# Performance work log

Hardware: AMD Instinct MI355X
Metric: run time of the kernel (lower is better)

## Reference

```python
import jax, jax.numpy as jnp
import numpy as np

B, T, D, N = 4, 1024, 1024, 16


def setup_inputs() -> dict:
    key = jax.random.key(0)
    ks = jax.random.split(key, 16)
    s = 1.0 / np.sqrt(D)
    inp = {
        "u": jax.random.normal(ks[0], (B, T, D), jnp.float32),
        "Win": jax.random.normal(ks[1], (D, D), jnp.float32) * s,
        "b_in": jnp.zeros((D,), jnp.float32),
        "Wg": jax.random.normal(ks[2], (D, D), jnp.float32) * s,
        "bg": jnp.zeros((D,), jnp.float32),
        "Wout": jax.random.normal(ks[3], (D, D), jnp.float32) * s,
        "bout": jnp.zeros((D,), jnp.float32),
        "convw": jax.random.normal(ks[4], (D, 3), jnp.float32) * 0.5,  # depthwise k=3
        "convb": jnp.zeros((D,), jnp.float32),
        "A": -jnp.exp(jax.random.normal(ks[5], (D, N), jnp.float32) * 0.5),  # negative diag
        "Wb": jax.random.normal(ks[6], (D, N), jnp.float32) * s,
        "bb": jnp.zeros((N,), jnp.float32),
        "Wc": jax.random.normal(ks[7], (D, N), jnp.float32) * s,
        "bc": jnp.zeros((N,), jnp.float32),
        "Wdt": jax.random.normal(ks[8], (D, D), jnp.float32) * s,
        "bdt": jnp.full((D,), -2.0, jnp.float32),  # small initial dt after softplus
    }
    return inp


def _depthwise_conv3_same(x, w, b):
    # x: [B,T,D], w: [D,3], b: [D]; Conv1d(k=3, padding=1, groups=D)
    xp = jnp.pad(x, ((0, 0), (1, 1), (0, 0)))
    return xp[:, :-2] * w[:, 0] + xp[:, 1:-1] * w[:, 1] + xp[:, 2:] * w[:, 2] + b


def _selective_scan(x, A, Wb, bb, Wc, bc, Wdt, bdt):
    # x: [B,T,D]
    dt = jax.nn.softplus(x @ Wdt + bdt)            # [B,T,D]
    Bm = x @ Wb + bb                               # [B,T,N]
    Cm = x @ Wc + bc                               # [B,T,N]
    dA = jnp.exp(dt[..., None] * A)                # [B,T,D,N]
    dBx = dt[..., None] * Bm[:, :, None, :] * x[..., None]  # [B,T,D,N]

    def step(h, ins):
        dA_t, dBx_t, C_t = ins                     # [B,D,N],[B,D,N],[B,N]
        h = dA_t * h + dBx_t
        y = jnp.einsum('bdn,bn->bd', h, C_t)
        return h, y

    h0 = jnp.zeros((x.shape[0], x.shape[2], A.shape[1]), x.dtype)
    _, ys = jax.lax.scan(
        step, h0,
        (dA.transpose(1, 0, 2, 3), dBx.transpose(1, 0, 2, 3), Cm.transpose(1, 0, 2)))
    return ys.transpose(1, 0, 2)                   # [B,T,D]


def reference(u, Win, b_in, Wg, bg, Wout, bout, convw, convb, A, Wb, bb, Wc, bc, Wdt, bdt):
    x = u @ Win + b_in                             # in_proj
    x = _depthwise_conv3_same(x, convw, convb)     # depthwise conv, same padding
    x = jax.nn.silu(x)
    x_ssm = _selective_scan(x, A, Wb, bb, Wc, bc, Wdt, bdt)
    z = jax.nn.silu(u @ Wg + bg)                   # gate
    return (x_ssm * z) @ Wout + bout
```

## Files before the change

### kernel.cpp

```cpp
#include <hip/hip_runtime.h>
#include <hip/hip_bf16.h>
#include <math.h>

#define BB 4
#define TT 1024
#define DD 1024
#define NNs 16
#define MM (BB*TT)
#define MMDD ((size_t)MM*DD)
#define CHUNK 64
#define NCHUNK (TT/CHUNK)

typedef short bf16x8 __attribute__((ext_vector_type(8)));
typedef float f32x4  __attribute__((ext_vector_type(4)));

__device__ __forceinline__ float silu_f(float v)     { return v / (1.f + __expf(-v)); }
__device__ __forceinline__ float softplus_f(float v) { return fmaxf(v, 0.f) + log1pf(__expf(-fabsf(v))); }

__device__ __forceinline__ unsigned short f2bf(float f) {
  unsigned u = __builtin_bit_cast(unsigned, f);
  u += 0x7fffu + ((u >> 16) & 1u);
  return (unsigned short)(u >> 16);
}
__device__ __forceinline__ unsigned pk2(float a, float b) {
  return (unsigned)f2bf(a) | ((unsigned)f2bf(b) << 16);
}

__device__ __forceinline__ void gload16(const void* g, void* l) {
  __builtin_amdgcn_global_load_lds(
      (const __attribute__((address_space(1))) unsigned*)g,
      (__attribute__((address_space(3))) unsigned*)l, 16, 0, 0);
}

__device__ __forceinline__ int2 xcd_swz(int gx) {
  int nwg  = gx * (int)gridDim.y;
  int orig = (int)blockIdx.y * gx + (int)blockIdx.x;
  int q = nwg >> 3, r = nwg & 7;
  int xcd = orig & 7, i = orig >> 3;
  int wg = (xcd < r ? xcd * (q + 1) : r * (q + 1) + (xcd - r) * q) + i;
  return make_int2(wg % gx, wg / gx);
}

__global__ __launch_bounds__(256) void wconv_t4(
    const float* __restrict__ W0, const float* __restrict__ W1,
    const float* __restrict__ W2, const float* __restrict__ W3,
    short* __restrict__ o0, short* __restrict__ o1,
    short* __restrict__ o2, short* __restrict__ o3)
{
  const float* W; short* Wt;
  switch (blockIdx.z) {
    case 0:  W = W0; Wt = o0; break;
    case 1:  W = W1; Wt = o1; break;
    case 2:  W = W2; Wt = o2; break;
    default: W = W3; Wt = o3; break;
  }
  __shared__ float t[32][33];
  int n0 = blockIdx.x * 32, k0 = blockIdx.y * 32;
  int r  = threadIdx.x >> 3;
  int c4 = (threadIdx.x & 7) * 4;
  float4 v = *(const float4*)(W + (size_t)(k0 + r) * DD + n0 + c4);
  t[r][c4+0] = v.x; t[r][c4+1] = v.y; t[r][c4+2] = v.z; t[r][c4+3] = v.w;
  __syncthreads();
  short q0 = (short)f2bf(t[c4+0][r]);
  short q1 = (short)f2bf(t[c4+1][r]);
  short q2 = (short)f2bf(t[c4+2][r]);
  short q3 = (short)f2bf(t[c4+3][r]);
  *(short4*)(Wt + (size_t)(n0 + r) * DD + k0 + c4) = make_short4(q0, q1, q2, q3);
}

__global__ __launch_bounds__(256) void wbc_t(
    const float* __restrict__ Wb, const float* __restrict__ Wc,
    short* __restrict__ Wbct)
{
  int idx = blockIdx.x * 256 + threadIdx.x;
  int k = idx & (DD - 1);
  int n = idx >> 10;
  const float* W = (n < 16) ? Wb : Wc;
  Wbct[(size_t)n * DD + k] = (short)f2bf(W[(size_t)k * NNs + (n & 15)]);
}

__global__ __launch_bounds__(256) void to_bf16(
    const float* __restrict__ in, short* __restrict__ out)
{
  size_t i = (size_t)(blockIdx.x * 256 + threadIdx.x) * 8;
  float4 a = *(const float4*)(in + i);
  float4 b = *(const float4*)(in + i + 4);
  *(uint4*)(out + i) = make_uint4(pk2(a.x,a.y), pk2(a.z,a.w),
                                  pk2(b.x,b.y), pk2(b.z,b.w));
}

__device__ __forceinline__ void gemm_core(
    const short* __restrict__ Ab, const short* __restrict__ Bt,
    const float* __restrict__ bias, float* __restrict__ C,
    int Nn, int K, int bm0, int bn0, int epi,
    short* As, short* Bs)
{
  const int tid  = threadIdx.x;
  const int lane = tid & 63;
  const int w    = tid >> 6;
  const int wm0  = (w >> 1) * 64;
  const int wn0  = (w & 1) * 64;

  const int srow = tid >> 3;
  const int scol = ((tid & 7) ^ ((tid >> 3) & 7)) << 3;

  const short* gA = Ab + (size_t)(bm0 + srow) * K + scol;
  const short* gB = Bt + (size_t)(bn0 + srow) * K + scol;
  char* ldsA = (char*)As;
  char* ldsB = (char*)Bs;
  const int wuni = w * 1024;

  f32x4 acc[4][4];
  const f32x4 zz = {0.f, 0.f, 0.f, 0.f};
  #pragma unroll
  for (int m = 0; m < 4; m++)
    #pragma unroll
    for (int n = 0; n < 4; n++) acc[m][n] = zz;

  const int fr  = lane & 15;
  const int ks  = (lane >> 4) << 3;
  const int swz = (fr & 7) << 3;

  const int NT = K >> 6;

  #pragma unroll
  for (int i = 0; i < 4; i++) {
    gload16(gA + (size_t)(i * 32) * K, ldsA + i * 4096 + wuni);
    gload16(gB + (size_t)(i * 32) * K, ldsB + i * 4096 + wuni);
  }
  __syncthreads();

  for (int t = 0; t < NT; ++t) {
    const int cur = t & 1;
    if (t + 1 < NT) {
      const int k1 = (t + 1) << 6;
      const int bo = (cur ^ 1) * 16384;
      #pragma unroll
      for (int i = 0; i < 4; i++) {
        gload16(gA + (size_t)(i * 32) * K + k1, ldsA + bo + i * 4096 + wuni);
        gload16(gB + (size_t)(i * 32) * K + k1, ldsB + bo + i * 4096 + wuni);
      }
    }
    const short* Ac = As + cur * 8192;
    const short* Bc = Bs + cur * 8192;
    #pragma unroll
    for (int s = 0; s < 2; s++) {
      const int cs = ((s << 5) | ks) ^ swz;
      bf16x8 af[4], bf[4];
      #pragma unroll
      for (int m = 0; m < 4; m++)
        af[m] = *(const bf16x8*)&Ac[(wm0 + m*16 + fr) * 64 + cs];
      #pragma unroll
      for (int n = 0; n < 4; n++)
        bf[n] = *(const bf16x8*)&Bc[(wn0 + n*16 + fr) * 64 + cs];
      #pragma unroll
      for (int m = 0; m < 4; m++)
        #pragma unroll
        for (int n = 0; n < 4; n++)
          acc[m][n] = __builtin_amdgcn_mfma_f32_16x16x32_bf16(af[m], bf[n], acc[m][n], 0, 0, 0);
    }
    __syncthreads();
  }

  const int orow = (lane >> 4) * 4;
  const int ocol = lane & 15;
  #pragma unroll
  for (int n = 0; n < 4; n++) {
    const int col = bn0 + wn0 + n*16 + ocol;
    const float bv = bias[col];
    #pragma unroll
    for (int m = 0; m < 4; m++) {
      #pragma unroll
      for (int r = 0; r < 4; r++) {
        float v = acc[m][n][r] + bv;
        if (epi == 1) v = silu_f(v);
        else if (epi == 2) v = softplus_f(v);
        C[(size_t)(bm0 + wm0 + m*16 + orow + r) * Nn + col] = v;
      }
    }
  }
}

__global__ __launch_bounds__(256) void gemm_bf16_k(
    const short* __restrict__ Ab, const short* __restrict__ Bt,
    const float* __restrict__ bias, float* __restrict__ C,
    int Nn, int K, int epi)
{
  __shared__ short As[2*128*64];
  __shared__ short Bs[2*128*64];
  int2 p = xcd_swz(gridDim.x);
  gemm_core(Ab, Bt, bias, C, Nn, K, p.y * 128, p.x * 128, epi, As, Bs);
}

__global__ __launch_bounds__(256) void gemm_ing_k(
    const short* __restrict__ ub,
    const short* __restrict__ Wti, const short* __restrict__ Wtg,
    const float* __restrict__ b_in, const float* __restrict__ bg,
    float* __restrict__ x1, float* __restrict__ z)
{
  __shared__ short As[2*128*64];
  __shared__ short Bs[2*128*64];
  int2 p = xcd_swz(gridDim.x);
  const int gate = p.x >> 3;
  gemm_core(ub, gate ? Wtg : Wti, gate ? bg : b_in, gate ? z : x1,
            DD, DD, p.y * 128, (p.x & 7) * 128, gate ? 1 : 0, As, Bs);
}

__global__ __launch_bounds__(256) void gemm_dtbc_k(
    const short* __restrict__ xb, const short* __restrict__ Wtd,
    const short* __restrict__ Wbct,
    const float* __restrict__ bdt, const float* __restrict__ bb,
    const float* __restrict__ bc,
    float* __restrict__ dt, float* __restrict__ Bm, float* __restrict__ Cm)
{
  __shared__ short As[2*128*64];
  __shared__ short Bs[2*128*64];
  __shared__ short Cs[2*32*64];
  int2 p = xcd_swz(gridDim.x);
  const int bx = p.x;
  const int bm0 = p.y * 128;
  const int bn0 = bx * 128;

  const int tid  = threadIdx.x;
  const int lane = tid & 63;
  const int w    = tid >> 6;
  const int wm0  = (w >> 1) * 64;
  const int wn0  = (w & 1) * 64;

  const int srow = tid >> 3;
  const int scol = ((tid & 7) ^ ((tid >> 3) & 7)) << 3;

  const short* gA = xb   + (size_t)(bm0 + srow) * DD + scol;
  const short* gB = Wtd  + (size_t)(bn0 + srow) * DD + scol;
  const short* gC = Wbct + (size_t)srow * DD + scol;
  char* ldsA = (char*)As;
  char* ldsB = (char*)Bs;
  char* ldsC = (char*)Cs;
  const int wuni = w * 1024;

  f32x4 acc[4][4];
  const f32x4 zz = {0.f, 0.f, 0.f, 0.f};
  #pragma unroll
  for (int m = 0; m < 4; m++)
    #pragma unroll
    for (int n = 0; n < 4; n++) acc[m][n] = zz;
  f32x4 accbc = zz;

  const int fr  = lane & 15;
  const int ks  = (lane >> 4) << 3;
  const int swz = (fr & 7) << 3;

  #pragma unroll
  for (int i = 0; i < 4; i++) {
    gload16(gA + (size_t)(i * 32) * DD, ldsA + i * 4096 + wuni);
    gload16(gB + (size_t)(i * 32) * DD, ldsB + i * 4096 + wuni);
  }
  gload16(gC, ldsC + wuni);
  __syncthreads();

  for (int t = 0; t < 16; ++t) {
    const int cur = t & 1;
    if (t + 1 < 16) {
      const int k1 = (t + 1) << 6;
      const int bo = (cur ^ 1) * 16384;
      #pragma unroll
      for (int i = 0; i < 4; i++) {
        gload16(gA + (size_t)(i * 32) * DD + k1, ldsA + bo + i * 4096 + wuni);
        gload16(gB + (size_t)(i * 32) * DD + k1, ldsB + bo + i * 4096 + wuni);
      }
      gload16(gC + k1, ldsC + (cur ^ 1) * 4096 + wuni);
    }
    const short* Ac = As + cur * 8192;
    const short* Bc = Bs + cur * 8192;
    const short* Cc = Cs + cur * 2048;
    #pragma unroll
    for (int s = 0; s < 2; s++) {
      const int cs = ((s << 5) | ks) ^ swz;
      bf16x8 af[4], bf[4];
      #pragma unroll
      for (int m = 0; m < 4; m++)
        af[m] = *(const bf16x8*)&Ac[(wm0 + m*16 + fr) * 64 + cs];
      #pragma unroll
      for (int n = 0; n < 4; n++)
        bf[n] = *(const bf16x8*)&Bc[(wn0 + n*16 + fr) * 64 + cs];
      #pragma unroll
      for (int m = 0; m < 4; m++)
        #pragma unroll
        for (int n = 0; n < 4; n++)
          acc[m][n] = __builtin_amdgcn_mfma_f32_16x16x32_bf16(af[m], bf[n], acc[m][n], 0, 0, 0);
      if (w < 2) {
        bf16x8 abc = *(const bf16x8*)&Ac[(bx*16 + fr) * 64 + cs];
        bf16x8 bbc = *(const bf16x8*)&Cc[((w << 4) + fr) * 64 + cs];
        accbc = __builtin_amdgcn_mfma_f32_16x16x32_bf16(abc, bbc, accbc, 0, 0, 0);
      }
    }
    __syncthreads();
  }

  const int orow = (lane >> 4) * 4;
  const int ocol = lane & 15;
  #pragma unroll
  for (int n = 0; n < 4; n++) {
    const int col = bn0 + wn0 + n*16 + ocol;
    const float bv = bdt[col];
    #pragma unroll
    for (int m = 0; m < 4; m++) {
      #pragma unroll
      for (int r = 0; r < 4; r++) {
        float v = acc[m][n][r] + bv;
        dt[(size_t)(bm0 + wm0 + m*16 + orow + r) * DD + col] = softplus_f(v);
      }
    }
  }
  if (w < 2) {
    const float bv = (w == 0 ? bb : bc)[ocol];
    float* dst = (w == 0) ? Bm : Cm;
    #pragma unroll
    for (int r = 0; r < 4; r++) {
      int row = bm0 + bx*16 + orow + r;
      dst[(size_t)row * NNs + ocol] = accbc[r] + bv;
    }
  }
}

__global__ __launch_bounds__(256) void conv_silu(
    const float* __restrict__ x1, const float* __restrict__ cw,
    const float* __restrict__ cb, float* __restrict__ x,
    short* __restrict__ xb)
{
  int idx = blockIdx.x * 256 + threadIdx.x;
  int d4 = idx & (DD/4 - 1);
  int bt = idx >> 8;
  int t  = bt & (TT - 1);
  const float4* b4 = (const float4*)x1;
  size_t ri = (size_t)bt * (DD/4) + d4;
  float4 zz = make_float4(0.f, 0.f, 0.f, 0.f);
  float4 vc = b4[ri];
  float4 vm = (t > 0)      ? b4[ri - DD/4] : zz;
  float4 vp = (t < TT - 1) ? b4[ri + DD/4] : zz;
  float rm[4] = {vm.x, vm.y, vm.z, vm.w};
  float rc[4] = {vc.x, vc.y, vc.z, vc.w};
  float rp[4] = {vp.x, vp.y, vp.z, vp.w};
  float o[4];
  #pragma unroll
  for (int j = 0; j < 4; j++) {
    int d = d4*4 + j;
    float v = rm[j]*cw[d*3+0] + rc[j]*cw[d*3+1] + rp[j]*cw[d*3+2] + cb[d];
    o[j] = silu_f(v);
  }
  ((float4*)x)[ri] = make_float4(o[0], o[1], o[2], o[3]);
  ((uint2*)xb)[ri] = make_uint2(pk2(o[0], o[1]), pk2(o[2], o[3]));
}

__global__ __launch_bounds__(256) void scan_local(
    const float* __restrict__ dt, const float* __restrict__ x,
    const float* __restrict__ Bm, const float* __restrict__ A,
    float* __restrict__ P, float* __restrict__ S)
{
  __shared__ float Bs[CHUNK*NNs];
  int bid = blockIdx.x;
  int dblk = bid & 3;
  int c = (bid >> 2) & 15;
  int b = bid >> 6;
  int d = dblk*256 + threadIdx.x;
  int t0 = c * CHUNK;
  for (int i = threadIdx.x; i < CHUNK*NNs; i += 256)
    Bs[i] = Bm[(size_t)(b*TT + t0)*NNs + i];
  float a[NNs];
  #pragma unroll
  for (int n = 0; n < NNs; n++) a[n] = A[d*NNs + n];
  __syncthreads();
  float h[NNs], p[NNs];
  #pragma unroll
  for (int n = 0; n < NNs; n++) { h[n] = 0.f; p[n] = 1.f; }
  size_t base = (size_t)(b*TT + t0)*DD + d;
  for (int tt = 0; tt < CHUNK; tt++) {
    float dtv = dt[base + (size_t)tt*DD];
    float xv  = x [base + (size_t)tt*DD];
    float dx = dtv * xv;
    #pragma unroll
    for (int n = 0; n < NNs; n++) {
      float e = __expf(dtv * a[n]);
      h[n] = fmaf(e, h[n], dx * Bs[tt*NNs + n]);
      p[n] *= e;
    }
  }
  size_t o = ((size_t)((b*NCHUNK + c)*DD + d)) * NNs;
  #pragma unroll
  for (int n = 0; n < NNs; n += 4) {
    *(float4*)&P[o+n] = make_float4(p[n], p[n+1], p[n+2], p[n+3]);
    *(float4*)&S[o+n] = make_float4(h[n], h[n+1], h[n+2], h[n+3]);
  }
}

__global__ __launch_bounds__(256) void scan_combine(
    const float* __restrict__ P, const float* __restrict__ S,
    float* __restrict__ H0)
{
  int g = blockIdx.x*256 + threadIdx.x;
  int n = g & 15; int d = (g >> 4) & 1023; int b = g >> 14;
  float h = 0.f;
  for (int c = 0; c < NCHUNK; c++) {
    size_t idx = ((size_t)((b*NCHUNK + c)*DD + d)) * NNs + n;
    H0[idx] = h;
    h = fmaf(P[idx], h, S[idx]);
  }
}

__global__ __launch_bounds__(256) void scan_y(
    const float* __restrict__ dt, const float* __restrict__ x,
    const float* __restrict__ Bm, const float* __restrict__ Cm,
    const float* __restrict__ A,  const float* __restrict__ H0,
    const float* __restrict__ z,  short* __restrict__ xsb)
{
  __shared__ float Bs[CHUNK*NNs];
  __shared__ float Cs[CHUNK*NNs];
  int bid = blockIdx.x;
  int dblk = bid & 3;
  int c = (bid >> 2) & 15;
  int b = bid >> 6;
  int d = dblk*256 + threadIdx.x;
  int t0 = c * CHUNK;
  for (int i = threadIdx.x; i < CHUNK*NNs; i += 256) {
    Bs[i] = Bm[(size_t)(b*TT + t0)*NNs + i];
    Cs[i] = Cm[(size_t)(b*TT + t0)*NNs + i];
  }
  float a[NNs];
  #pragma unroll
  for (int n = 0; n < NNs; n++) a[n] = A[d*NNs + n];
  size_t ho = ((size_t)((b*NCHUNK + c)*DD + d)) * NNs;
  float h[NNs];
  #pragma unroll
  for (int n = 0; n < NNs; n += 4) {
    float4 h4 = *(const float4*)&H0[ho+n];
    h[n] = h4.x; h[n+1] = h4.y; h[n+2] = h4.z; h[n+3] = h4.w;
  }
  __syncthreads();
  size_t base = (size_t)(b*TT + t0)*DD + d;
  for (int tt = 0; tt < CHUNK; tt++) {
    float dtv = dt[base + (size_t)tt*DD];
    float xv  = x [base + (size_t)tt*DD];
    float dx = dtv * xv;
    float y = 0.f;
    #pragma unroll
    for (int n = 0; n < NNs; n++) {
      float e = __expf(dtv * a[n]);
      h[n] = fmaf(e, h[n], dx * Bs[tt*NNs + n]);
      y = fmaf(h[n], Cs[tt*NNs + n], y);
    }
    size_t gi = base + (size_t)tt*DD;
    xsb[gi] = (short)f2bf(y * z[gi]);
  }
}

extern "C" void kernel_launch(void* const* d_in, const int* in_sizes, int n_in,
                              void* d_out, int out_size, void* d_ws, size_t ws_size,
                              hipStream_t stream)
{
  const float* u     = (const float*)d_in[0];
  const float* Win   = (const float*)d_in[1];
  const float* b_in  = (const float*)d_in[2];
  const float* Wg    = (const float*)d_in[3];
  const float* bg    = (const float*)d_in[4];
  const float* Wout  = (const float*)d_in[5];
  const float* bout  = (const float*)d_in[6];
  const float* convw = (const float*)d_in[7];
  const float* convb = (const float*)d_in[8];
  const float* A     = (const float*)d_in[9];
  const float* Wb    = (const float*)d_in[10];
  const float* bb    = (const float*)d_in[11];
  const float* Wc    = (const float*)d_in[12];
  const float* bc    = (const float*)d_in[13];
  const float* Wdt   = (const float*)d_in[14];
  const float* bdt   = (const float*)d_in[15];
  float* out = (float*)d_out;

  float* ws = (float*)d_ws;
  float* x1 = ws;
  float* z  = x1 + MMDD;
  float* x  = z  + MMDD;
  float* dt = x  + MMDD;
  float* Bm = dt + MMDD;
  float* Cm = Bm + (size_t)MM*NNs;
  short* ub  = (short*)(Cm + (size_t)MM*NNs);
  short* xb  = ub  + MMDD;
  short* Wti = xb  + MMDD;
  short* Wtg = Wti + (size_t)DD*DD;
  short* Wtd = Wtg + (size_t)DD*DD;
  short* Wto = Wtd + (size_t)DD*DD;
  short* Wbct = Wto + (size_t)DD*DD;
  float* P  = x1;
  float* S  = P + (size_t)BB*NCHUNK*DD*NNs;
  float* H0 = S + (size_t)BB*NCHUNK*DD*NNs;
  short* xsb = ub;

  wconv_t4<<<dim3(DD/32, DD/32, 4), 256, 0, stream>>>(
      Win, Wg, Wdt, Wout, Wti, Wtg, Wtd, Wto);
  wbc_t<<<(32*DD)/256, 256, 0, stream>>>(Wb, Wc, Wbct);
  to_bf16<<<(MMDD/8)/256, 256, 0, stream>>>(u, ub);

  gemm_ing_k<<<dim3(16, MM/128), 256, 0, stream>>>(ub, Wti, Wtg, b_in, bg, x1, z);
  conv_silu<<<(MMDD/4)/256, 256, 0, stream>>>(x1, convw, convb, x, xb);
  gemm_dtbc_k<<<dim3(8, MM/128), 256, 0, stream>>>(
      xb, Wtd, Wbct, bdt, bb, bc, dt, Bm, Cm);
  scan_local  <<<BB*NCHUNK*(DD/256), 256, 0, stream>>>(dt, x, Bm, A, P, S);
  scan_combine<<<(BB*DD*NNs)/256,    256, 0, stream>>>(P, S, H0);
  scan_y      <<<BB*NCHUNK*(DD/256), 256, 0, stream>>>(dt, x, Bm, Cm, A, H0, z, xsb);
  gemm_bf16_k<<<dim3(8, MM/128), 256, 0, stream>>>(xsb, Wto, bout, out, DD, DD, 0);
}
```

Measured before the change: 308.0 us.

## Triple-buffer GEMM LDS stages with vmcnt waits and one barrier per tile

Moves the bf16 GEMM kernels from double to triple LDS buffering, issuing loads two K-tiles ahead. Each iteration now does a partial s_waitcnt on vmcnt and a single s_barrier instead of two __syncthreads. The goal is to hide more global-to-LDS load latency and cut barrier stalls. In exchange, LDS use per block grows by half, which may lower occupancy, and correctness depends on the vmcnt counts matching the number of outstanding loads.

```diff
diff --git a/kernel.cpp b/kernel.cpp
--- a/kernel.cpp
+++ b/kernel.cpp
@@ -123,26 +123,27 @@
 
   const int NT = K >> 6;
 
-  #pragma unroll
-  for (int i = 0; i < 4; i++) {
-    gload16(gA + (size_t)(i * 32) * K, ldsA + i * 4096 + wuni);
-    gload16(gB + (size_t)(i * 32) * K, ldsB + i * 4096 + wuni);
-  }
-  __syncthreads();
+  auto STAGE = [&](int t) {
+    const int ko = t << 6;
+    const int bo = (t % 3) * 16384;
+    #pragma unroll
+    for (int i = 0; i < 4; i++) {
+      gload16(gA + (size_t)(i * 32) * K + ko, ldsA + bo + i * 4096 + wuni);
+      gload16(gB + (size_t)(i * 32) * K + ko, ldsB + bo + i * 4096 + wuni);
+    }
+  };
+
+  STAGE(0);
+  STAGE(1);
 
   for (int t = 0; t < NT; ++t) {
-    const int cur = t & 1;
-    if (t + 1 < NT) {
-      const int k1 = (t + 1) << 6;
-      const int bo = (cur ^ 1) * 16384;
-      #pragma unroll
-      for (int i = 0; i < 4; i++) {
-        gload16(gA + (size_t)(i * 32) * K + k1, ldsA + bo + i * 4096 + wuni);
-        gload16(gB + (size_t)(i * 32) * K + k1, ldsB + bo + i * 4096 + wuni);
-      }
-    }
-    const short* Ac = As + cur * 8192;
-    const short* Bc = Bs + cur * 8192;
+    if (t + 1 < NT) asm volatile("s_waitcnt vmcnt(8)" ::: "memory");
+    else            asm volatile("s_waitcnt vmcnt(0)" ::: "memory");
+    __builtin_amdgcn_s_barrier();
+    if (t + 2 < NT) STAGE(t + 2);
+
+    const short* Ac = As + (t % 3) * 8192;
+    const short* Bc = Bs + (t % 3) * 8192;
     #pragma unroll
     for (int s = 0; s < 2; s++) {
       const int cs = ((s << 5) | ks) ^ swz;
@@ -159,7 +160,6 @@
         for (int n = 0; n < 4; n++)
           acc[m][n] = __builtin_amdgcn_mfma_f32_16x16x32_bf16(af[m], bf[n], acc[m][n], 0, 0, 0);
     }
-    __syncthreads();
   }
 
   const int orow = (lane >> 4) * 4;
@@ -186,8 +186,8 @@
     const float* __restrict__ bias, float* __restrict__ C,
     int Nn, int K, int epi)
 {
-  __shared__ short As[2*128*64];
-  __shared__ short Bs[2*128*64];
+  __shared__ short As[3*128*64];
+  __shared__ short Bs[3*128*64];
   int2 p = xcd_swz(gridDim.x);
   gemm_core(Ab, Bt, bias, C, Nn, K, p.y * 128, p.x * 128, epi, As, Bs);
 }
@@ -198,8 +198,8 @@
     const float* __restrict__ b_in, const float* __restrict__ bg,
     float* __restrict__ x1, float* __restrict__ z)
 {
-  __shared__ short As[2*128*64];
-  __shared__ short Bs[2*128*64];
+  __shared__ short As[3*128*64];
+  __shared__ short Bs[3*128*64];
   int2 p = xcd_swz(gridDim.x);
   const int gate = p.x >> 3;
   gemm_core(ub, gate ? Wtg : Wti, gate ? bg : b_in, gate ? z : x1,
@@ -213,11 +213,11 @@
     const float* __restrict__ bc,
     float* __restrict__ dt, float* __restrict__ Bm, float* __restrict__ Cm)
 {
-  __shared__ short As[2*128*64];
-  __shared__ short Bs[2*128*64];
-  __shared__ short Cs[2*32*64];
+  __shared__ short As[3*128*64];
+  __shared__ short Bs[3*128*64];
+  __shared__ short Cs[3*32*64];
   int2 p = xcd_swz(gridDim.x);
-  const int bx = p.x;
+  const int bx  = p.x;
   const int bm0 = p.y * 128;
   const int bn0 = bx * 128;
 
@@ -250,29 +250,29 @@
   const int ks  = (lane >> 4) << 3;
   const int swz = (fr & 7) << 3;
 
-  #pragma unroll
-  for (int i = 0; i < 4; i++) {
-    gload16(gA + (size_t)(i * 32) * DD, ldsA + i * 4096 + wuni);
-    gload16(gB + (size_t)(i * 32) * DD, ldsB + i * 4096 + wuni);
-  }
-  gload16(gC, ldsC + wuni);
-  __syncthreads();
+  auto STAGE = [&](int t) {
+    const int ko = t << 6;
+    const int bo = (t % 3) * 16384;
+    #pragma unroll
+    for (int i = 0; i < 4; i++) {
+      gload16(gA + (size_t)(i * 32) * DD + ko, ldsA + bo + i * 4096 + wuni);
+      gload16(gB + (size_t)(i * 32) * DD + ko, ldsB + bo + i * 4096 + wuni);
+    }
+    gload16(gC + ko, ldsC + (t % 3) * 4096 + wuni);
+  };
+
+  STAGE(0);
+  STAGE(1);
 
   for (int t = 0; t < 16; ++t) {
-    const int cur = t & 1;
-    if (t + 1 < 16) {
-      const int k1 = (t + 1) << 6;
-      const int bo = (cur ^ 1) * 16384;
-      #pragma unroll
-      for (int i = 0; i < 4; i++) {
-        gload16(gA + (size_t)(i * 32) * DD + k1, ldsA + bo + i * 4096 + wuni);
-        gload16(gB + (size_t)(i * 32) * DD + k1, ldsB + bo + i * 4096 + wuni);
-      }
-      gload16(gC + k1, ldsC + (cur ^ 1) * 4096 + wuni);
-    }
-    const short* Ac = As + cur * 8192;
-    const short* Bc = Bs + cur * 8192;
-    const short* Cc = Cs + cur * 2048;
+    if (t + 1 < 16) asm volatile("s_waitcnt vmcnt(9)" ::: "memory");
+    else            asm volatile("s_waitcnt vmcnt(0)" ::: "memory");
+    __builtin_amdgcn_s_barrier();
+    if (t + 2 < 16) STAGE(t + 2);
+
+    const short* Ac = As + (t % 3) * 8192;
+    const short* Bc = Bs + (t % 3) * 8192;
+    const short* Cc = Cs + (t % 3) * 2048;
     #pragma unroll
     for (int s = 0; s < 2; s++) {
       const int cs = ((s << 5) | ks) ^ swz;
@@ -294,7 +294,6 @@
         accbc = __builtin_amdgcn_mfma_f32_16x16x32_bf16(abc, bbc, accbc, 0, 0, 0);
       }
     }
-    __syncthreads();
   }
 
   const int orow = (lane >> 4) * 4;
```

Result: slower. 317.4 us (+3.0%).

## Split-K the dt/BC and output GEMMs and fuse bias/softplus into scans

Applied to the files above, without the earlier changes.

The dt/B/C GEMM and the output GEMM now split K in two halves across blockIdx.z, doubling the number of workgroups from 256 to 512 so more compute units are filled. Partial sums are written to separate buffers. The scan kernels combine them and apply bias and softplus on the fly, and a new epilogue kernel adds the two output partials plus bias. The fp32 copy of x is dropped and the scans read the bf16 x instead, which cuts memory traffic but lowers the precision of x in the scan. In exchange there is an extra partial-buffer write and read for dt and the output, plus one more launch.

```diff
diff --git a/kernel.cpp b/kernel.cpp
--- a/kernel.cpp
+++ b/kernel.cpp
@@ -24,6 +24,9 @@
 }
 __device__ __forceinline__ unsigned pk2(float a, float b) {
   return (unsigned)f2bf(a) | ((unsigned)f2bf(b) << 16);
+}
+__device__ __forceinline__ float bf2f(short s) {
+  return __builtin_bit_cast(float, ((unsigned)(unsigned short)s) << 16);
 }
 
 __device__ __forceinline__ void gload16(const void* g, void* l) {
@@ -92,7 +95,7 @@
 __device__ __forceinline__ void gemm_core(
     const short* __restrict__ Ab, const short* __restrict__ Bt,
     const float* __restrict__ bias, float* __restrict__ C,
-    int Nn, int K, int bm0, int bn0, int epi,
+    int Nn, int K, int kBase, int kLen, int bm0, int bn0, int epi,
     short* As, short* Bs)
 {
   const int tid  = threadIdx.x;
@@ -104,8 +107,8 @@
   const int srow = tid >> 3;
   const int scol = ((tid & 7) ^ ((tid >> 3) & 7)) << 3;
 
-  const short* gA = Ab + (size_t)(bm0 + srow) * K + scol;
-  const short* gB = Bt + (size_t)(bn0 + srow) * K + scol;
+  const short* gA = Ab + (size_t)(bm0 + srow) * K + kBase + scol;
+  const short* gB = Bt + (size_t)(bn0 + srow) * K + kBase + scol;
   char* ldsA = (char*)As;
   char* ldsB = (char*)Bs;
   const int wuni = w * 1024;
@@ -121,7 +124,7 @@
   const int ks  = (lane >> 4) << 3;
   const int swz = (fr & 7) << 3;
 
-  const int NT = K >> 6;
+  const int NT = kLen >> 6;
 
   #pragma unroll
   for (int i = 0; i < 4; i++) {
@@ -167,7 +170,7 @@
   #pragma unroll
   for (int n = 0; n < 4; n++) {
     const int col = bn0 + wn0 + n*16 + ocol;
-    const float bv = bias[col];
+    const float bv = bias ? bias[col] : 0.f;
     #pragma unroll
     for (int m = 0; m < 4; m++) {
       #pragma unroll
@@ -181,17 +184,6 @@
   }
 }
 
-__global__ __launch_bounds__(256) void gemm_bf16_k(
-    const short* __restrict__ Ab, const short* __restrict__ Bt,
-    const float* __restrict__ bias, float* __restrict__ C,
-    int Nn, int K, int epi)
-{
-  __shared__ short As[2*128*64];
-  __shared__ short Bs[2*128*64];
-  int2 p = xcd_swz(gridDim.x);
-  gemm_core(Ab, Bt, bias, C, Nn, K, p.y * 128, p.x * 128, epi, As, Bs);
-}
-
 __global__ __launch_bounds__(256) void gemm_ing_k(
     const short* __restrict__ ub,
     const short* __restrict__ Wti, const short* __restrict__ Wtg,
@@ -203,23 +195,40 @@
   int2 p = xcd_swz(gridDim.x);
   const int gate = p.x >> 3;
   gemm_core(ub, gate ? Wtg : Wti, gate ? bg : b_in, gate ? z : x1,
-            DD, DD, p.y * 128, (p.x & 7) * 128, gate ? 1 : 0, As, Bs);
+            DD, DD, 0, DD, p.y * 128, (p.x & 7) * 128, gate ? 1 : 0, As, Bs);
+}
+
+__global__ __launch_bounds__(256) void gemm_out_k(
+    const short* __restrict__ xsb, const short* __restrict__ Wto,
+    float* __restrict__ O0, float* __restrict__ O1)
+{
+  __shared__ short As[2*128*64];
+  __shared__ short Bs[2*128*64];
+  int2 p = xcd_swz(gridDim.x);
+  const int s = blockIdx.z;
+  gemm_core(xsb, Wto, nullptr, s ? O1 : O0,
+            DD, DD, s * 512, 512, p.y * 128, p.x * 128, 0, As, Bs);
 }
 
 __global__ __launch_bounds__(256) void gemm_dtbc_k(
     const short* __restrict__ xb, const short* __restrict__ Wtd,
     const short* __restrict__ Wbct,
-    const float* __restrict__ bdt, const float* __restrict__ bb,
-    const float* __restrict__ bc,
-    float* __restrict__ dt, float* __restrict__ Bm, float* __restrict__ Cm)
+    float* __restrict__ d0, float* __restrict__ d1,
+    float* __restrict__ B0, float* __restrict__ B1,
+    float* __restrict__ C0, float* __restrict__ C1)
 {
   __shared__ short As[2*128*64];
   __shared__ short Bs[2*128*64];
   __shared__ short Cs[2*32*64];
   int2 p = xcd_swz(gridDim.x);
-  const int bx = p.x;
+  const int sp  = blockIdx.z;
+  const int kB  = sp * 512;
+  const int bx  = p.x;
   const int bm0 = p.y * 128;
   const int bn0 = bx * 128;
+  float* dOut = sp ? d1 : d0;
+  float* bOut = sp ? B1 : B0;
+  float* cOut = sp ? C1 : C0;
 
   const int tid  = threadIdx.x;
   const int lane = tid & 63;
@@ -230,9 +239,9 @@
   const int srow = tid >> 3;
   const int scol = ((tid & 7) ^ ((tid >> 3) & 7)) << 3;
 
-  const short* gA = xb   + (size_t)(bm0 + srow) * DD + scol;
-  const short* gB = Wtd  + (size_t)(bn0 + srow) * DD + scol;
-  const short* gC = Wbct + (size_t)srow * DD + scol;
+  const short* gA = xb   + (size_t)(bm0 + srow) * DD + kB + scol;
+  const short* gB = Wtd  + (size_t)(bn0 + srow) * DD + kB + scol;
+  const short* gC = Wbct + (size_t)srow * DD + kB + scol;
   char* ldsA = (char*)As;
   char* ldsB = (char*)Bs;
   char* ldsC = (char*)Cs;
@@ -258,9 +267,9 @@
   gload16(gC, ldsC + wuni);
   __syncthreads();
 
-  for (int t = 0; t < 16; ++t) {
+  for (int t = 0; t < 8; ++t) {
     const int cur = t & 1;
-    if (t + 1 < 16) {
+    if (t + 1 < 8) {
       const int k1 = (t + 1) << 6;
       const int bo = (cur ^ 1) * 16384;
       #pragma unroll
@@ -302,31 +311,26 @@
   #pragma unroll
   for (int n = 0; n < 4; n++) {
     const int col = bn0 + wn0 + n*16 + ocol;
-    const float bv = bdt[col];
     #pragma unroll
     for (int m = 0; m < 4; m++) {
       #pragma unroll
-      for (int r = 0; r < 4; r++) {
-        float v = acc[m][n][r] + bv;
-        dt[(size_t)(bm0 + wm0 + m*16 + orow + r) * DD + col] = softplus_f(v);
-      }
+      for (int r = 0; r < 4; r++)
+        dOut[(size_t)(bm0 + wm0 + m*16 + orow + r) * DD + col] = acc[m][n][r];
     }
   }
   if (w < 2) {
-    const float bv = (w == 0 ? bb : bc)[ocol];
-    float* dst = (w == 0) ? Bm : Cm;
+    float* dst = (w == 0) ? bOut : cOut;
     #pragma unroll
     for (int r = 0; r < 4; r++) {
       int row = bm0 + bx*16 + orow + r;
-      dst[(size_t)row * NNs + ocol] = accbc[r] + bv;
+      dst[(size_t)row * NNs + ocol] = accbc[r];
     }
   }
 }
 
 __global__ __launch_bounds__(256) void conv_silu(
     const float* __restrict__ x1, const float* __restrict__ cw,
-    const float* __restrict__ cb, float* __restrict__ x,
-    short* __restrict__ xb)
+    const float* __restrict__ cb, short* __restrict__ xb)
 {
   int idx = blockIdx.x * 256 + threadIdx.x;
   int d4 = idx & (DD/4 - 1);
@@ -348,40 +352,44 @@
     float v = rm[j]*cw[d*3+0] + rc[j]*cw[d*3+1] + rp[j]*cw[d*3+2] + cb[d];
     o[j] = silu_f(v);
   }
-  ((float4*)x)[ri] = make_float4(o[0], o[1], o[2], o[3]);
   ((uint2*)xb)[ri] = make_uint2(pk2(o[0], o[1]), pk2(o[2], o[3]));
 }
 
 __global__ __launch_bounds__(256) void scan_local(
-    const float* __restrict__ dt, const float* __restrict__ x,
-    const float* __restrict__ Bm, const float* __restrict__ A,
+    const float* __restrict__ d0, const float* __restrict__ d1,
+    const float* __restrict__ bdt, const short* __restrict__ xb,
+    const float* __restrict__ B0, const float* __restrict__ B1,
+    const float* __restrict__ bb, const float* __restrict__ A,
     float* __restrict__ P, float* __restrict__ S)
 {
-  __shared__ float Bs[CHUNK*NNs];
+  __shared__ float Bsh[CHUNK*NNs];
   int bid = blockIdx.x;
   int dblk = bid & 3;
   int c = (bid >> 2) & 15;
   int b = bid >> 6;
   int d = dblk*256 + threadIdx.x;
   int t0 = c * CHUNK;
+  size_t bo = (size_t)(b*TT + t0)*NNs;
   for (int i = threadIdx.x; i < CHUNK*NNs; i += 256)
-    Bs[i] = Bm[(size_t)(b*TT + t0)*NNs + i];
+    Bsh[i] = B0[bo + i] + B1[bo + i] + bb[i & 15];
   float a[NNs];
   #pragma unroll
   for (int n = 0; n < NNs; n++) a[n] = A[d*NNs + n];
+  const float bdtv = bdt[d];
   __syncthreads();
   float h[NNs], p[NNs];
   #pragma unroll
   for (int n = 0; n < NNs; n++) { h[n] = 0.f; p[n] = 1.f; }
   size_t base = (size_t)(b*TT + t0)*DD + d;
   for (int tt = 0; tt < CHUNK; tt++) {
-    float dtv = dt[base + (size_t)tt*DD];
-    float xv  = x [base + (size_t)tt*DD];
+    size_t gi = base + (size_t)tt*DD;
+    float dtv = softplus_f(d0[gi] + d1[gi] + bdtv);
+    float xv  = bf2f(xb[gi]);
     float dx = dtv * xv;
     #pragma unroll
     for (int n = 0; n < NNs; n++) {
       float e = __expf(dtv * a[n]);
-      h[n] = fmaf(e, h[n], dx * Bs[tt*NNs + n]);
+      h[n] = fmaf(e, h[n], dx * Bsh[tt*NNs + n]);
       p[n] *= e;
     }
   }
@@ -402,32 +410,39 @@
   float h = 0.f;
   for (int c = 0; c < NCHUNK; c++) {
     size_t idx = ((size_t)((b*NCHUNK + c)*DD + d)) * NNs + n;
+    float pv = P[idx], sv = S[idx];
     H0[idx] = h;
-    h = fmaf(P[idx], h, S[idx]);
+    h = fmaf(pv, h, sv);
   }
 }
 
 __global__ __launch_bounds__(256) void scan_y(
-    const float* __restrict__ dt, const float* __restrict__ x,
-    const float* __restrict__ Bm, const float* __restrict__ Cm,
+    const float* __restrict__ d0, const float* __restrict__ d1,
+    const float* __restrict__ bdt, const short* __restrict__ xb,
+    const float* __restrict__ B0, const float* __restrict__ B1,
+    const float* __restrict__ bb,
+    const float* __restrict__ C0, const float* __restrict__ C1,
+    const float* __restrict__ bc,
     const float* __restrict__ A,  const float* __restrict__ H0,
     const float* __restrict__ z,  short* __restrict__ xsb)
 {
-  __shared__ float Bs[CHUNK*NNs];
-  __shared__ float Cs[CHUNK*NNs];
+  __shared__ float Bsh[CHUNK*NNs];
+  __shared__ float Csh[CHUNK*NNs];
   int bid = blockIdx.x;
   int dblk = bid & 3;
   int c = (bid >> 2) & 15;
   int b = bid >> 6;
   int d = dblk*256 + threadIdx.x;
   int t0 = c * CHUNK;
+  size_t bo = (size_t)(b*TT + t0)*NNs;
   for (int i = threadIdx.x; i < CHUNK*NNs; i += 256) {
-    Bs[i] = Bm[(size_t)(b*TT + t0)*NNs + i];
-    Cs[i] = Cm[(size_t)(b*TT + t0)*NNs + i];
+    Bsh[i] = B0[bo + i] + B1[bo + i] + bb[i & 15];
+    Csh[i] = C0[bo + i] + C1[bo + i] + bc[i & 15];
   }
   float a[NNs];
   #pragma unroll
   for (int n = 0; n < NNs; n++) a[n] = A[d*NNs + n];
+  const float bdtv = bdt[d];
   size_t ho = ((size_t)((b*NCHUNK + c)*DD + d)) * NNs;
   float h[NNs];
   #pragma unroll
@@ -438,19 +453,32 @@
   __syncthreads();
   size_t base = (size_t)(b*TT + t0)*DD + d;
   for (int tt = 0; tt < CHUNK; tt++) {
-    float dtv = dt[base + (size_t)tt*DD];
-    float xv  = x [base + (size_t)tt*DD];
+    size_t gi = base + (size_t)tt*DD;
+    float dtv = softplus_f(d0[gi] + d1[gi] + bdtv);
+    float xv  = bf2f(xb[gi]);
     float dx = dtv * xv;
     float y = 0.f;
     #pragma unroll
     for (int n = 0; n < NNs; n++) {
       float e = __expf(dtv * a[n]);
-      h[n] = fmaf(e, h[n], dx * Bs[tt*NNs + n]);
-      y = fmaf(h[n], Cs[tt*NNs + n], y);
-    }
-    size_t gi = base + (size_t)tt*DD;
+      h[n] = fmaf(e, h[n], dx * Bsh[tt*NNs + n]);
+      y = fmaf(h[n], Csh[tt*NNs + n], y);
+    }
     xsb[gi] = (short)f2bf(y * z[gi]);
   }
+}
+
+__global__ __launch_bounds__(256) void out_epi(
+    const float* __restrict__ O0, const float* __restrict__ O1,
+    const float* __restrict__ bout, float* __restrict__ out)
+{
+  size_t i = (size_t)(blockIdx.x * 256 + threadIdx.x) * 4;
+  int col = (int)(i & (DD - 1));
+  float4 a = *(const float4*)(O0 + i);
+  float4 b = *(const float4*)(O1 + i);
+  float4 bv = *(const float4*)(bout + col);
+  *(float4*)(out + i) = make_float4(a.x + b.x + bv.x, a.y + b.y + bv.y,
+                                    a.z + b.z + bv.z, a.w + b.w + bv.w);
 }
 
 extern "C" void kernel_launch(void* const* d_in, const int* in_sizes, int n_in,
@@ -478,11 +506,13 @@
   float* ws = (float*)d_ws;
   float* x1 = ws;
   float* z  = x1 + MMDD;
-  float* x  = z  + MMDD;
-  float* dt = x  + MMDD;
-  float* Bm = dt + MMDD;
-  float* Cm = Bm + (size_t)MM*NNs;
-  short* ub  = (short*)(Cm + (size_t)MM*NNs);
+  float* d0 = z  + MMDD;
+  float* d1 = d0 + MMDD;
+  float* B0 = d1 + MMDD;
+  float* B1 = B0 + (size_t)MM*NNs;
+  float* C0 = B1 + (size_t)MM*NNs;
+  float* C1 = C0 + (size_t)MM*NNs;
+  short* ub  = (short*)(C1 + (size_t)MM*NNs);
   short* xb  = ub  + MMDD;
   short* Wti = xb  + MMDD;
   short* Wtg = Wti + (size_t)DD*DD;
@@ -491,7 +521,9 @@
   short* Wbct = Wto + (size_t)DD*DD;
   float* P  = x1;
   float* S  = P + (size_t)BB*NCHUNK*DD*NNs;
-  float* H0 = S + (size_t)BB*NCHUNK*DD*NNs;
+  float* H0 = P;
+  float* O0 = d0;
+  float* O1 = d1;
   short* xsb = ub;
 
   wconv_t4<<<dim3(DD/32, DD/32, 4), 256, 0, stream>>>(
@@ -500,11 +532,14 @@
   to_bf16<<<(MMDD/8)/256, 256, 0, stream>>>(u, ub);
 
   gemm_ing_k<<<dim3(16, MM/128), 256, 0, stream>>>(ub, Wti, Wtg, b_in, bg, x1, z);
-  conv_silu<<<(MMDD/4)/256, 256, 0, stream>>>(x1, convw, convb, x, xb);
-  gemm_dtbc_k<<<dim3(8, MM/128), 256, 0, stream>>>(
-      xb, Wtd, Wbct, bdt, bb, bc, dt, Bm, Cm);
-  scan_local  <<<BB*NCHUNK*(DD/256), 256, 0, stream>>>(dt, x, Bm, A, P, S);
-  scan_combine<<<(BB*DD*NNs)/256,    256, 0, stream>>>(P, S, H0);
-  scan_y      <<<BB*NCHUNK*(DD/256), 256, 0, stream>>>(dt, x, Bm, Cm, A, H0, z, xsb);
-  gemm_bf16_k<<<dim3(8, MM/128), 256, 0, stream>>>(xsb, Wto, bout, out, DD, DD, 0);
-}
+  conv_silu<<<(MMDD/4)/256, 256, 0, stream>>>(x1, convw, convb, xb);
+  gemm_dtbc_k<<<dim3(8, MM/128, 2), 256, 0, stream>>>(
+      xb, Wtd, Wbct, d0, d1, B0, B1, C0, C1);
+  scan_local  <<<BB*NCHUNK*(DD/256), 256, 0, stream>>>(
+      d0, d1, bdt, xb, B0, B1, bb, A, P, S);
+  scan_combine<<<(BB*DD*NNs)/256, 256, 0, stream>>>(P, S, H0);
+  scan_y      <<<BB*NCHUNK*(DD/256), 256, 0, stream>>>(
+      d0, d1, bdt, xb, B0, B1, bb, C0, C1, bc, A, H0, z, xsb);
+  gemm_out_k<<<dim3(8, MM/128, 2), 256, 0, stream>>>(xsb, Wto, O0, O1);
+  out_epi<<<(MMDD/4)/256, 256, 0, stream>>>(O0, O1, bout, out);
+}
```

After: 297.4 us. 1.04x faster.
